# Kernel optimization log

Hardware: AMD Instinct MI355X
Metric: run time of the kernel (lower is better)

Reference implementation:

```python
import jax, jax.numpy as jnp
import numpy as np

B, H, W, D, O = 16, 128, 128, 64, 256

def setup_inputs() -> dict:
    key = jax.random.key(0)
    k1, k2 = jax.random.split(key)
    x = jax.random.normal(k1, (B, H, W, D), dtype=jnp.float32)
    omega = jax.random.normal(k2, (O, D), dtype=jnp.float32)  # prototypes, init N(0,1)
    return {"x": x, "omega": omega}

def reference(x, omega):
    # Squared L2 distance from each pixel feature to each prototype,
    x2 = jnp.sum(x * x, axis=-1, keepdims=True)          # [B,H,W,1]
    p2 = jnp.sum(omega * omega, axis=-1)                  # [O]
    xp = jnp.einsum('bhwd,od->bhwo', x, omega)            # [B,H,W,O]
    dist = x2 + p2 - 2.0 * xp                             # [B,H,W,O]
    # original stacks per-prototype [B,H,W,1] slices along dim=3 -> [B,H,W,O,1]
    return dist[..., None]
```

## Files before the change

kernel.cpp:

```cpp
#include <hip/hip_runtime.h>


typedef __attribute__((ext_vector_type(4))) float f32x4;
typedef __attribute__((ext_vector_type(16))) float f32x16;
typedef __attribute__((ext_vector_type(8))) short s16x8;

constexpr int D_ = 64;
constexpr int O_ = 256;
constexpr int M_ = 16 * 128 * 128;
constexpr int ITERS = 8;
constexpr int PIX_PER_ITER = 32;
constexpr int PIX_PER_BLOCK = ITERS * PIX_PER_ITER;
constexpr int NBLOCKS = M_ / PIX_PER_BLOCK;
constexpr int LROW = 68;

__device__ __forceinline__ unsigned short f2bf(float f) {
    unsigned u = __builtin_bit_cast(unsigned, f);
    u += 0x7FFFu + ((u >> 16) & 1u);
    return (unsigned short)(u >> 16);
}

#define LDS_BARRIER() do {                                        \
    asm volatile("s_waitcnt lgkmcnt(0)" ::: "memory");            \
    __builtin_amdgcn_sched_barrier(0);                            \
    __builtin_amdgcn_s_barrier();                                 \
    __builtin_amdgcn_sched_barrier(0);                            \
} while (0)

__global__ __launch_bounds__(256, 4) void dist_kernel(
    const float* __restrict__ x,
    const float* __restrict__ om,
    float* __restrict__ out)
{
    __shared__ float xstg[3][32 * LROW];

    const int tid  = threadIdx.x;
    const int wave = tid >> 6;
    const int lane = tid & 63;
    const int p    = lane & 31;
    const int h    = lane >> 5;

    s16x8 Bf0[4], Bf1[4];
    float p2r0 = 0.f, p2r1 = 0.f;
#pragma unroll
    for (int tt = 0; tt < 2; ++tt) {
        const int T = wave * 2 + tt;
        float p2p = 0.f;
#pragma unroll
        for (int s = 0; s < 4; ++s) {
            const float* src = om + (T * 32 + p) * D_ + s * 16 + h * 8;
            f32x4 v0 = *(const f32x4*)(src);
            f32x4 v1 = *(const f32x4*)(src + 4);
            s16x8 f;
#pragma unroll
            for (int j = 0; j < 4; ++j) {
                f[j]     = (short)f2bf(v0[j]); p2p += v0[j] * v0[j];
                f[4 + j] = (short)f2bf(v1[j]); p2p += v1[j] * v1[j];
            }
            if (tt == 0) Bf0[s] = f; else Bf1[s] = f;
        }
        p2p += __shfl_xor(p2p, 32);
        if (tt == 0) p2r0 = p2p; else p2r1 = p2p;
    }

    const size_t gbase = (size_t)blockIdx.x * PIX_PER_BLOCK * D_;
    const int sr = tid >> 4;
    const int sc = (tid & 15) * 4;

    f32x4 nva0, nva1, nvb0, nvb1;
    {
        const float* s0 = x + gbase + tid * 4;
        f32x4 t0 = __builtin_nontemporal_load((const f32x4*)(s0));
        f32x4 t1 = __builtin_nontemporal_load((const f32x4*)(s0 + 1024));
        const float* s1 = x + gbase + 2048 + tid * 4;
        nvb0 = __builtin_nontemporal_load((const f32x4*)(s1));
        nvb1 = __builtin_nontemporal_load((const f32x4*)(s1 + 1024));
        *(f32x4*)&xstg[0][sr * LROW + sc] = t0;
        *(f32x4*)&xstg[0][(16 + sr) * LROW + sc] = t1;
    }
    __syncthreads();

#pragma unroll
    for (int it = 0; it < ITERS; ++it) {
        const int rbase = blockIdx.x * PIX_PER_BLOCK + it * PIX_PER_ITER;

        if (it + 2 < ITERS) {
            const float* s = x + gbase + (size_t)(it + 2) * (PIX_PER_ITER * D_) + tid * 4;
            if ((it & 1) == 0) {
                nva0 = __builtin_nontemporal_load((const f32x4*)(s));
                nva1 = __builtin_nontemporal_load((const f32x4*)(s + 1024));
            } else {
                nvb0 = __builtin_nontemporal_load((const f32x4*)(s));
                nvb1 = __builtin_nontemporal_load((const f32x4*)(s + 1024));
            }
        }

        const float* row = &xstg[it % 3][p * LROW + h * 8];
        s16x8 Af[4];
        float x2p = 0.f;
#pragma unroll
        for (int s = 0; s < 4; ++s) {
            f32x4 a0 = *(const f32x4*)(row + s * 16);
            f32x4 a1 = *(const f32x4*)(row + s * 16 + 4);
#pragma unroll
            for (int j = 0; j < 4; ++j) {
                Af[s][j]     = (short)f2bf(a0[j]); x2p += a0[j] * a0[j];
                Af[s][4 + j] = (short)f2bf(a1[j]); x2p += a1[j] * a1[j];
            }
        }
        x2p += __shfl_xor(x2p, 32);

        f32x16 acc0 = {0.f, 0.f, 0.f, 0.f, 0.f, 0.f, 0.f, 0.f,
                       0.f, 0.f, 0.f, 0.f, 0.f, 0.f, 0.f, 0.f};
        f32x16 acc1 = acc0;
#pragma unroll
        for (int s = 0; s < 4; ++s) {
            acc0 = __builtin_amdgcn_mfma_f32_32x32x16_bf16(Af[s], Bf0[s], acc0, 0, 0, 0);
            acc1 = __builtin_amdgcn_mfma_f32_32x32x16_bf16(Af[s], Bf1[s], acc1, 0, 0, 0);
        }

        if (it + 1 < ITERS) {
            float* dst = &xstg[(it + 1) % 3][0];
            if (((it + 1) & 1) == 0) {
                *(f32x4*)&dst[sr * LROW + sc] = nva0;
                *(f32x4*)&dst[(16 + sr) * LROW + sc] = nva1;
            } else {
                *(f32x4*)&dst[sr * LROW + sc] = nvb0;
                *(f32x4*)&dst[(16 + sr) * LROW + sc] = nvb1;
            }
            LDS_BARRIER();
        }

        const int T0 = wave * 2;
        float* const ob0 = out + (size_t)(rbase + 4 * h) * O_ + T0 * 32 + p;
#pragma unroll
        for (int reg = 0; reg < 16; ++reg) {
            const int r = (reg & 3) + 8 * (reg >> 2);
            const float x2v = __shfl(x2p, r + 4 * h);
            ob0[(size_t)r * O_]      = (x2v + p2r0) - 2.f * acc0[reg];
            ob0[(size_t)r * O_ + 32] = (x2v + p2r1) - 2.f * acc1[reg];
        }
    }
}

extern "C" void kernel_launch(void* const* d_in, const int* in_sizes, int n_in,
                              void* d_out, int out_size, void* d_ws, size_t ws_size,
                              hipStream_t stream) {
    const float* x  = (const float*)d_in[0];
    const float* om = (const float*)d_in[1];
    float* out = (float*)d_out;

    dist_kernel<<<dim3(NBLOCKS), dim3(256), 0, stream>>>(x, om, out);
}
```

Before: 67.60 us.

## Stage x tiles with direct global-to-LDS loads and an XOR-swizzled layout

Replaces the register-staged prefetch of x (global load into VGPRs, then ds_write) with global_load_lds, which writes straight into a triple-buffered LDS ring. The padded row layout is dropped in favour of an XOR swizzle on the column index to avoid bank conflicts. Barriers now rely on hand-counted vmcnt waits that account for outstanding output stores. This removes the VGPR round trip and the LDS write instructions, but correctness depends on the exact vmcnt values and on how the hardware orders the stores.

```diff
diff --git a/kernel.cpp b/kernel.cpp
--- a/kernel.cpp
+++ b/kernel.cpp
@@ -12,7 +12,6 @@
 constexpr int PIX_PER_ITER = 32;
 constexpr int PIX_PER_BLOCK = ITERS * PIX_PER_ITER;
 constexpr int NBLOCKS = M_ / PIX_PER_BLOCK;
-constexpr int LROW = 68;
 
 __device__ __forceinline__ unsigned short f2bf(float f) {
     unsigned u = __builtin_bit_cast(unsigned, f);
@@ -20,19 +19,12 @@
     return (unsigned short)(u >> 16);
 }
 
-#define LDS_BARRIER() do {                                        \
-    asm volatile("s_waitcnt lgkmcnt(0)" ::: "memory");            \
-    __builtin_amdgcn_sched_barrier(0);                            \
-    __builtin_amdgcn_s_barrier();                                 \
-    __builtin_amdgcn_sched_barrier(0);                            \
-} while (0)
-
 __global__ __launch_bounds__(256, 4) void dist_kernel(
     const float* __restrict__ x,
     const float* __restrict__ om,
     float* __restrict__ out)
 {
-    __shared__ float xstg[3][32 * LROW];
+    __shared__ float xstg[3][2048];
 
     const int tid  = threadIdx.x;
     const int wave = tid >> 6;
@@ -64,44 +56,44 @@
     }
 
     const size_t gbase = (size_t)blockIdx.x * PIX_PER_BLOCK * D_;
-    const int sr = tid >> 4;
-    const int sc = (tid & 15) * 4;
 
-    f32x4 nva0, nva1, nvb0, nvb1;
-    {
-        const float* s0 = x + gbase + tid * 4;
-        f32x4 t0 = __builtin_nontemporal_load((const f32x4*)(s0));
-        f32x4 t1 = __builtin_nontemporal_load((const f32x4*)(s0 + 1024));
-        const float* s1 = x + gbase + 2048 + tid * 4;
-        nvb0 = __builtin_nontemporal_load((const f32x4*)(s1));
-        nvb1 = __builtin_nontemporal_load((const f32x4*)(s1 + 1024));
-        *(f32x4*)&xstg[0][sr * LROW + sc] = t0;
-        *(f32x4*)&xstg[0][(16 + sr) * LROW + sc] = t1;
-    }
-    __syncthreads();
+    auto stage = [&](int tile, int buf) {
+#pragma unroll
+        for (int k = 0; k < 2; ++k) {
+            const int r = wave * 8 + k * 4 + (lane >> 4);
+            const int c = ((lane & 15) * 4) ^ (8 * (r & 7));
+            const float* src = x + gbase + (size_t)tile * (PIX_PER_ITER * D_)
+                                 + r * 64 + c;
+            __builtin_amdgcn_global_load_lds(
+                (const __attribute__((address_space(1))) unsigned int*)(const void*)src,
+                (__attribute__((address_space(3))) unsigned int*)(void*)
+                    &xstg[buf][wave * 512 + k * 256],
+                16, 0, 2 );
+        }
+    };
+
+    stage(0, 0);
+    stage(1, 1);
+    asm volatile("s_waitcnt vmcnt(2)" ::: "memory");
+    __builtin_amdgcn_sched_barrier(0);
+    __builtin_amdgcn_s_barrier();
+    __builtin_amdgcn_sched_barrier(0);
 
 #pragma unroll
     for (int it = 0; it < ITERS; ++it) {
         const int rbase = blockIdx.x * PIX_PER_BLOCK + it * PIX_PER_ITER;
 
-        if (it + 2 < ITERS) {
-            const float* s = x + gbase + (size_t)(it + 2) * (PIX_PER_ITER * D_) + tid * 4;
-            if ((it & 1) == 0) {
-                nva0 = __builtin_nontemporal_load((const f32x4*)(s));
-                nva1 = __builtin_nontemporal_load((const f32x4*)(s + 1024));
-            } else {
-                nvb0 = __builtin_nontemporal_load((const f32x4*)(s));
-                nvb1 = __builtin_nontemporal_load((const f32x4*)(s + 1024));
-            }
-        }
+        if (it + 2 < ITERS) stage(it + 2, (it + 2) % 3);
 
-        const float* row = &xstg[it % 3][p * LROW + h * 8];
+        const float* rowb = &xstg[it % 3][p * 64];
+        const int xm = 8 * (p & 7);
         s16x8 Af[4];
         float x2p = 0.f;
 #pragma unroll
         for (int s = 0; s < 4; ++s) {
-            f32x4 a0 = *(const f32x4*)(row + s * 16);
-            f32x4 a1 = *(const f32x4*)(row + s * 16 + 4);
+            const int idx = (h * 8 + s * 16) ^ xm;
+            f32x4 a0 = *(const f32x4*)&rowb[idx];
+            f32x4 a1 = *(const f32x4*)&rowb[idx + 4];
 #pragma unroll
             for (int j = 0; j < 4; ++j) {
                 Af[s][j]     = (short)f2bf(a0[j]); x2p += a0[j] * a0[j];
@@ -120,15 +112,13 @@
         }
 
         if (it + 1 < ITERS) {
-            float* dst = &xstg[(it + 1) % 3][0];
-            if (((it + 1) & 1) == 0) {
-                *(f32x4*)&dst[sr * LROW + sc] = nva0;
-                *(f32x4*)&dst[(16 + sr) * LROW + sc] = nva1;
-            } else {
-                *(f32x4*)&dst[sr * LROW + sc] = nvb0;
-                *(f32x4*)&dst[(16 + sr) * LROW + sc] = nvb1;
-            }
-            LDS_BARRIER();
+            if (it == 0)             asm volatile("s_waitcnt vmcnt(2)"  ::: "memory");
+            else if (it + 2 < ITERS) asm volatile("s_waitcnt vmcnt(34)" ::: "memory");
+            else                     asm volatile("s_waitcnt vmcnt(32)" ::: "memory");
+            asm volatile("s_waitcnt lgkmcnt(0)" ::: "memory");
+            __builtin_amdgcn_sched_barrier(0);
+            __builtin_amdgcn_s_barrier();
+            __builtin_amdgcn_sched_barrier(0);
         }
 
         const int T0 = wave * 2;
```

Result: faster. 64.38 us (-4.8%).
